# Performance work log

Hardware: AMD Instinct MI355X
Metric: run time of the kernel (lower is better)

The kernel has to match this reference:

```python
import jax, jax.numpy as jnp
import numpy as np

B, LS, LH, D1, D2 = 16, 1024, 1024, 1024, 1024


def setup_inputs() -> dict:
    key = jax.random.key(0)
    k1, k2, k3 = jax.random.split(key, 3)
    S = jax.random.normal(k1, (B, LS, D1), dtype=jnp.float32)
    H = jax.random.normal(k2, (B, LH, D2), dtype=jnp.float32)
    pad_mask = jnp.zeros((B, LS, LH), dtype=jnp.float32)  # additive mask
    W_w = jax.random.normal(k3, (D2, D1), dtype=jnp.float32) / np.sqrt(D1)
    W_b = jnp.zeros((D2,), dtype=jnp.float32)
    return {"S": S, "H": H, "pad_mask": pad_mask, "W_w": W_w, "W_b": W_b}


def reference(S, H, pad_mask, W_w, W_b):
    # Linear projection: S_ = S @ W^T + b  -> [B, LS, D2]
    S_ = jnp.einsum('bsd,ed->bse', S, W_w) + W_b
    # Unscaled dot-product scores: [B, LS, LH]
    score = jnp.einsum('bse,bte->bst', S_, H)
    score = score + pad_mask  # additive pad mask
    score = jax.nn.softmax(score, axis=-1)
    # Weighted sum of H: [B, LS, D2]
    out = jnp.einsum('bst,bte->bse', score, H)
    return out
```

## Files before the change

### kernel.cpp

```cpp
#include <hip/hip_runtime.h>
#include <stdint.h>

typedef _Float16 half8 __attribute__((ext_vector_type(8)));
typedef float floatx4 __attribute__((ext_vector_type(4)));

__device__ __forceinline__ uint16_t f16bits(_Float16 h) {
  union { _Float16 f; uint16_t u; } x; x.f = h; return x.u;
}

__device__ __forceinline__ void g2l16(const void* g, void* l) {
  __builtin_amdgcn_global_load_lds((const __attribute__((address_space(1))) void*)g,
                                   (__attribute__((address_space(3))) void*)l,
                                   16, 0, 0);
}

__global__ __launch_bounds__(256) void split_f16_kernel(
    const float* __restrict__ x, uint16_t* __restrict__ hi,
    uint16_t* __restrict__ lo, int n4) {
  int i = blockIdx.x * 256 + threadIdx.x;
  if (i >= n4) return;
  float4 v = ((const float4*)x)[i];
  ushort4 h, l;
  _Float16 a;
  a = (_Float16)v.x; h.x = f16bits(a); l.x = f16bits((_Float16)(v.x - (float)a));
  a = (_Float16)v.y; h.y = f16bits(a); l.y = f16bits((_Float16)(v.y - (float)a));
  a = (_Float16)v.z; h.z = f16bits(a); l.z = f16bits((_Float16)(v.z - (float)a));
  a = (_Float16)v.w; h.w = f16bits(a); l.w = f16bits((_Float16)(v.w - (float)a));
  ((ushort4*)hi)[i] = h;
  ((ushort4*)lo)[i] = l;
}

__global__ __launch_bounds__(256) void split_h_kernel(
    const float* __restrict__ src, uint16_t* __restrict__ hi,
    uint16_t* __restrict__ lo, uint16_t* __restrict__ ht) {
  __shared__ uint16_t tile[64][65];
  const int e0 = blockIdx.x * 64;
  const int t0 = blockIdx.y * 64;
  const size_t bb = (size_t)blockIdx.z << 20;
  const int r = threadIdx.x >> 4;
  const int c = (threadIdx.x & 15) * 4;
#pragma unroll
  for (int it = 0; it < 4; ++it) {
    const int tr = r + it * 16;
    const size_t idx = bb + (size_t)(t0 + tr) * 1024 + e0 + c;
    float4 v = *(const float4*)(src + idx);
    ushort4 h, l;
    _Float16 a;
    a = (_Float16)v.x; h.x = f16bits(a); l.x = f16bits((_Float16)(v.x - (float)a));
    a = (_Float16)v.y; h.y = f16bits(a); l.y = f16bits((_Float16)(v.y - (float)a));
    a = (_Float16)v.z; h.z = f16bits(a); l.z = f16bits((_Float16)(v.z - (float)a));
    a = (_Float16)v.w; h.w = f16bits(a); l.w = f16bits((_Float16)(v.w - (float)a));
    *(ushort4*)(hi + idx) = h;
    *(ushort4*)(lo + idx) = l;
    tile[c + 0][tr] = h.x;
    tile[c + 1][tr] = h.y;
    tile[c + 2][tr] = h.z;
    tile[c + 3][tr] = h.w;
  }
  __syncthreads();
#pragma unroll
  for (int it = 0; it < 4; ++it) {
    const int er = r + it * 16;
    ushort4 o;
    o.x = tile[er][c + 0];
    o.y = tile[er][c + 1];
    o.z = tile[er][c + 2];
    o.w = tile[er][c + 3];
    *(ushort4*)(ht + bb + (size_t)(e0 + er) * 1024 + t0 + c) = o;
  }
}

template <bool SPLIT, int MODE, int GMAP>
__global__ __launch_bounds__(256, 4) void gemm_bt(
    const uint16_t* __restrict__ Ahi, const uint16_t* __restrict__ Alo,
    const uint16_t* __restrict__ Bhi, const uint16_t* __restrict__ Blo,
    uint16_t* __restrict__ Chi, uint16_t* __restrict__ Clo,
    float* __restrict__ Cf, const float* __restrict__ mask,
    const float* __restrict__ bias, int N, int K,
    long batchA, long batchB, long batchC) {
  constexpr int NBUF = SPLIT ? 2 : 1;
  constexpr int LOI = SPLIT ? 1 : 0;
  __shared__ __align__(16) uint16_t sA[2][NBUF][128 * 32];
  __shared__ __align__(16) uint16_t sB[NBUF][128 * 32];

  const int tid = threadIdx.x;
  const int lane = tid & 63;
  const int w = tid >> 6;
  const int wr = w >> 1, wc = w & 1;
  const int quad = lane >> 4, l16 = lane & 15;

  int m_t, n_t, z;
  if constexpr (GMAP == 0) {
    m_t = blockIdx.x; n_t = blockIdx.y; z = 0;
  } else {
    z = blockIdx.x; m_t = blockIdx.y >> 3; n_t = blockIdx.y & 7;
  }
  const int m0 = m_t * 128;
  const int n0 = n_t * 128;
  const size_t zA = (size_t)z * batchA;
  const size_t zB = (size_t)z * batchB;
  const size_t zC = (size_t)z * batchC;

  const int r0 = w * 32 + (lane >> 2);
  const int ldc =
      (((lane & 3) ^ ((lane >> 2) & 3) ^ (((lane >> 4) & 1) << 1)) * 16);

  const char* gAh0 = (const char*)(Ahi + zA + (size_t)(m0 + r0) * K) + ldc;
  const char* gAh1 = gAh0 + (size_t)16 * K * 2;
  const char* gBh0 = (const char*)(Bhi + zB + (size_t)(n0 + r0) * K) + ldc;
  const char* gBh1 = gBh0 + (size_t)16 * K * 2;
  const char* gAl0 = gAh0; const char* gAl1 = gAh1;
  const char* gBl0 = gBh0; const char* gBl1 = gBh1;
  if constexpr (SPLIT) {
    gAl0 = (const char*)(Alo + zA + (size_t)(m0 + r0) * K) + ldc;
    gAl1 = gAl0 + (size_t)16 * K * 2;
    gBl0 = (const char*)(Blo + zB + (size_t)(n0 + r0) * K) + ldc;
    gBl1 = gBl0 + (size_t)16 * K * 2;
  }

  auto stageA = [&](int buf, int kt) {
    const int kb = kt * 64;
    g2l16(gAh0 + kb, &sA[buf][0][(w * 32) * 32]);
    g2l16(gAh1 + kb, &sA[buf][0][(w * 32 + 16) * 32]);
    if constexpr (SPLIT) {
      g2l16(gAl0 + kb, &sA[buf][LOI][(w * 32) * 32]);
      g2l16(gAl1 + kb, &sA[buf][LOI][(w * 32 + 16) * 32]);
    }
  };
  auto stageB = [&](int kt) {
    const int kb = kt * 64;
    g2l16(gBh0 + kb, &sB[0][(w * 32) * 32]);
    g2l16(gBh1 + kb, &sB[0][(w * 32 + 16) * 32]);
    if constexpr (SPLIT) {
      g2l16(gBl0 + kb, &sB[LOI][(w * 32) * 32]);
      g2l16(gBl1 + kb, &sB[LOI][(w * 32 + 16) * 32]);
    }
  };

  const int key = (l16 & 3) ^ (((l16 >> 2) & 1) << 1);
  const int aoff = (wr * 64 + l16) * 32 + ((quad ^ key) * 8);
  const int boff = (wc * 64 + l16) * 32 + ((quad ^ key) * 8);

  floatx4 acc[4][4];
  floatx4 zero = {0.f, 0.f, 0.f, 0.f};
#pragma unroll
  for (int i = 0; i < 4; ++i)
#pragma unroll
    for (int j = 0; j < 4; ++j) acc[i][j] = zero;

  const int nkt = K >> 5;
  stageA(0, 0);
  asm volatile("s_waitcnt vmcnt(0)" ::: "memory");
  __builtin_amdgcn_s_barrier();
  asm volatile("" ::: "memory");

  int cur = 0;
  for (int kt = 0; kt < nkt; ++kt) {
    stageB(kt);
    const bool pre = (kt + 1 < nkt);
    if (pre) stageA(cur ^ 1, kt + 1);

    half8 fa[4];
#pragma unroll
    for (int i = 0; i < 4; ++i) fa[i] = *(const half8*)&sA[cur][0][aoff + i * 512];

    if (pre) {
      if constexpr (SPLIT)
        asm volatile("s_waitcnt vmcnt(4)" ::: "memory");
      else
        asm volatile("s_waitcnt vmcnt(2)" ::: "memory");
    } else {
      asm volatile("s_waitcnt vmcnt(0)" ::: "memory");
    }
    __builtin_amdgcn_s_barrier();
    asm volatile("" ::: "memory");

    if constexpr (SPLIT) {
      half8 fbl[4];
#pragma unroll
      for (int j = 0; j < 4; ++j) fbl[j] = *(const half8*)&sB[1][boff + j * 512];
#pragma unroll
      for (int i = 0; i < 4; ++i)
#pragma unroll
        for (int j = 0; j < 4; ++j)
          acc[i][j] = __builtin_amdgcn_mfma_f32_16x16x32_f16(fa[i], fbl[j], acc[i][j], 0, 0, 0);
    }
    half8 fbh[4];
#pragma unroll
    for (int j = 0; j < 4; ++j) fbh[j] = *(const half8*)&sB[0][boff + j * 512];
#pragma unroll
    for (int i = 0; i < 4; ++i)
#pragma unroll
      for (int j = 0; j < 4; ++j)
        acc[i][j] = __builtin_amdgcn_mfma_f32_16x16x32_f16(fa[i], fbh[j], acc[i][j], 0, 0, 0);
    if constexpr (SPLIT) {
      half8 fal[4];
#pragma unroll
      for (int i = 0; i < 4; ++i) fal[i] = *(const half8*)&sA[cur][1][aoff + i * 512];
#pragma unroll
      for (int i = 0; i < 4; ++i)
#pragma unroll
        for (int j = 0; j < 4; ++j)
          acc[i][j] = __builtin_amdgcn_mfma_f32_16x16x32_f16(fal[i], fbh[j], acc[i][j], 0, 0, 0);
    }
    __syncthreads();
    cur ^= 1;
  }

  const int crow0 = m0 + wr * 64 + quad * 4;
  const int ccol0 = n0 + wc * 64 + l16;
#pragma unroll
  for (int j = 0; j < 4; ++j) {
    const int col = ccol0 + j * 16;
    float bj = 0.f;
    if constexpr (MODE == 0) bj = bias[col];
#pragma unroll
    for (int i = 0; i < 4; ++i) {
#pragma unroll
      for (int r = 0; r < 4; ++r) {
        const int row = crow0 + i * 16 + r;
        const size_t idx = zC + (size_t)row * N + col;
        float v = acc[i][j][r];
        if constexpr (MODE == 0) {
          v += bj;
          _Float16 h = (_Float16)v;
          Chi[idx] = f16bits(h);
          Clo[idx] = f16bits((_Float16)(v - (float)h));
        } else if constexpr (MODE == 1) {
          Cf[idx] = v + mask[idx];
        } else {
          Cf[idx] = v;
        }
      }
    }
  }
}

__global__ __launch_bounds__(256, 2) void gemm_bt_k64(
    const uint16_t* __restrict__ A, const uint16_t* __restrict__ B,
    float* __restrict__ Cf, int N, int K,
    long batchA, long batchB, long batchC) {
  __shared__ __align__(16) uint16_t sA[2][128 * 64];
  __shared__ __align__(16) uint16_t sB[2][128 * 64];

  const int tid = threadIdx.x;
  const int lane = tid & 63;
  const int w = tid >> 6;
  const int wr = w >> 1, wc = w & 1;
  const int quad = lane >> 4, l16 = lane & 15;

  const int z = blockIdx.x;
  const int m_t = blockIdx.y >> 3, n_t = blockIdx.y & 7;
  const int m0 = m_t * 128, n0 = n_t * 128;
  const size_t zA = (size_t)z * batchA;
  const size_t zB = (size_t)z * batchB;
  const size_t zC = (size_t)z * batchC;

  const int r0 = w * 32 + (lane >> 3);
  const int ldc = (((lane & 7) ^ ((lane >> 3) & 7)) * 16);
  const size_t rowskip = (size_t)8 * K * 2;

  const char* gA = (const char*)(A + zA + (size_t)(m0 + r0) * K) + ldc;
  const char* gB = (const char*)(B + zB + (size_t)(n0 + r0) * K) + ldc;

  auto stage = [&](int buf, int kt) {
    const int kb = kt * 128;
#pragma unroll
    for (int it = 0; it < 4; ++it) {
      g2l16(gA + it * rowskip + kb, &sA[buf][(w * 32 + it * 8) * 64]);
      g2l16(gB + it * rowskip + kb, &sB[buf][(w * 32 + it * 8) * 64]);
    }
  };

  const int key = l16 & 7;
  const int arow = wr * 64 + l16;
  const int brow = wc * 64 + l16;

  floatx4 acc[4][4];
  floatx4 zero = {0.f, 0.f, 0.f, 0.f};
#pragma unroll
  for (int i = 0; i < 4; ++i)
#pragma unroll
    for (int j = 0; j < 4; ++j) acc[i][j] = zero;

  const int nkt = K >> 6;
  stage(0, 0);
  __syncthreads();
  int cur = 0;
  for (int kt = 0; kt < nkt; ++kt) {
    if (kt + 1 < nkt) stage(cur ^ 1, kt + 1);
#pragma unroll
    for (int kh = 0; kh < 2; ++kh) {
      const int co = (((kh << 2) | quad) ^ key) * 8;
      half8 fa[4], fb[4];
#pragma unroll
      for (int i = 0; i < 4; ++i)
        fa[i] = *(const half8*)&sA[cur][(arow + 16 * i) * 64 + co];
#pragma unroll
      for (int j = 0; j < 4; ++j)
        fb[j] = *(const half8*)&sB[cur][(brow + 16 * j) * 64 + co];
#pragma unroll
      for (int i = 0; i < 4; ++i)
#pragma unroll
        for (int j = 0; j < 4; ++j)
          acc[i][j] = __builtin_amdgcn_mfma_f32_16x16x32_f16(fa[i], fb[j], acc[i][j], 0, 0, 0);
    }
    __syncthreads();
    cur ^= 1;
  }

  const int crow0 = m0 + wr * 64 + quad * 4;
  const int ccol0 = n0 + wc * 64 + l16;
#pragma unroll
  for (int j = 0; j < 4; ++j) {
    const int col = ccol0 + j * 16;
#pragma unroll
    for (int i = 0; i < 4; ++i) {
#pragma unroll
      for (int r = 0; r < 4; ++r) {
        const int row = crow0 + i * 16 + r;
        Cf[zC + (size_t)row * N + col] = acc[i][j][r];
      }
    }
  }
}

__global__ __launch_bounds__(256) void softmax_kernel(
    const float* __restrict__ sc, uint16_t* __restrict__ p) {
  const int row = blockIdx.x;
  const float* x = sc + (size_t)row * 1024;
  const int t = threadIdx.x;
  float4 v = ((const float4*)x)[t];
  float m = fmaxf(fmaxf(v.x, v.y), fmaxf(v.z, v.w));
#pragma unroll
  for (int off = 32; off; off >>= 1) m = fmaxf(m, __shfl_xor(m, off));
  __shared__ float redm[4];
  __shared__ float reds[4];
  const int wv = t >> 6, ln = t & 63;
  if (ln == 0) redm[wv] = m;
  __syncthreads();
  m = fmaxf(fmaxf(redm[0], redm[1]), fmaxf(redm[2], redm[3]));
  float e0 = __expf(v.x - m), e1 = __expf(v.y - m);
  float e2 = __expf(v.z - m), e3 = __expf(v.w - m);
  float s = e0 + e1 + e2 + e3;
#pragma unroll
  for (int off = 32; off; off >>= 1) s += __shfl_xor(s, off);
  if (ln == 0) reds[wv] = s;
  __syncthreads();
  s = reds[0] + reds[1] + reds[2] + reds[3];
  float inv = 1.f / s;
  ushort4 o;
  o.x = f16bits((_Float16)(e0 * inv));
  o.y = f16bits((_Float16)(e1 * inv));
  o.z = f16bits((_Float16)(e2 * inv));
  o.w = f16bits((_Float16)(e3 * inv));
  ((ushort4*)(p + (size_t)row * 1024))[t] = o;
}

__global__ __launch_bounds__(256) void transpose_f16_kernel(
    const float* __restrict__ src, uint16_t* __restrict__ dst) {
  __shared__ uint16_t tile[64][65];
  const int e0 = blockIdx.x * 64;
  const int t0 = blockIdx.y * 64;
  const size_t bb = (size_t)blockIdx.z << 20;
  const int r = threadIdx.x >> 4;
  const int c = (threadIdx.x & 15) * 4;
#pragma unroll
  for (int it = 0; it < 4; ++it) {
    const int tr = r + it * 16;
    float4 v = *(const float4*)(src + bb + (size_t)(t0 + tr) * 1024 + e0 + c);
    tile[c + 0][tr] = f16bits((_Float16)v.x);
    tile[c + 1][tr] = f16bits((_Float16)v.y);
    tile[c + 2][tr] = f16bits((_Float16)v.z);
    tile[c + 3][tr] = f16bits((_Float16)v.w);
  }
  __syncthreads();
#pragma unroll
  for (int it = 0; it < 4; ++it) {
    const int er = r + it * 16;
    ushort4 o;
    o.x = tile[er][c + 0];
    o.y = tile[er][c + 1];
    o.z = tile[er][c + 2];
    o.w = tile[er][c + 3];
    *(ushort4*)(dst + bb + (size_t)(e0 + er) * 1024 + t0 + c) = o;
  }
}

extern "C" void kernel_launch(void* const* d_in, const int* in_sizes, int n_in,
                              void* d_out, int out_size, void* d_ws, size_t ws_size,
                              hipStream_t stream) {
  (void)in_sizes; (void)n_in; (void)out_size;
  const float* S    = (const float*)d_in[0];
  const float* H    = (const float*)d_in[1];
  const float* mask = (const float*)d_in[2];
  const float* Ww   = (const float*)d_in[3];
  const float* Wb   = (const float*)d_in[4];
  float* out = (float*)d_out;
  char* ws = (char*)d_ws;
  const size_t MB = 1024ull * 1024ull;

  uint16_t* Whi  = (uint16_t*)(ws + 0 * MB);
  uint16_t* Wlo  = (uint16_t*)(ws + 2 * MB);
  uint16_t* Pjhi = (uint16_t*)(ws + 4 * MB);
  uint16_t* Pjlo = (uint16_t*)(ws + 36 * MB);
  uint16_t* Hhi  = (uint16_t*)(ws + 68 * MB);
  uint16_t* Hlo  = (uint16_t*)(ws + 100 * MB);
  uint16_t* Shi  = (uint16_t*)(ws + 132 * MB);
  uint16_t* Slo  = (uint16_t*)(ws + 164 * MB);
  float*    SC   = (float*)(ws + 132 * MB);
  uint16_t* PR   = (uint16_t*)(ws + 68 * MB);

  const bool roomy = ws_size >= 229ull * MB;
  uint16_t* HT = roomy ? (uint16_t*)(ws + 196 * MB)
                       : (uint16_t*)(ws + 100 * MB);

  split_f16_kernel<<<16384, 256, 0, stream>>>(S, Shi, Slo, 4 * 1024 * 1024);
  split_f16_kernel<<<1024, 256, 0, stream>>>(Ww, Whi, Wlo, 256 * 1024);
  if (roomy) {
    split_h_kernel<<<dim3(16, 16, 16), 256, 0, stream>>>(H, Hhi, Hlo, HT);
  } else {
    split_f16_kernel<<<16384, 256, 0, stream>>>(H, Hhi, Hlo, 4 * 1024 * 1024);
  }

  gemm_bt<true, 0, 0><<<dim3(128, 8, 1), 256, 0, stream>>>(
      Shi, Slo, Whi, Wlo, Pjhi, Pjlo, nullptr, nullptr, Wb,
      1024, 1024, 0, 0, 0);
  gemm_bt<true, 1, 1><<<dim3(16, 64, 1), 256, 0, stream>>>(
      Pjhi, Pjlo, Hhi, Hlo, nullptr, nullptr, SC, mask, nullptr,
      1024, 1024, 1048576, 1048576, 1048576);
  softmax_kernel<<<16384, 256, 0, stream>>>(SC, PR);
  if (!roomy) {
    transpose_f16_kernel<<<dim3(16, 16, 16), 256, 0, stream>>>(H, HT);
  }
  gemm_bt_k64<<<dim3(16, 64, 1), 256, 0, stream>>>(
      PR, HT, out, 1024, 1024, 1048576, 1048576, 1048576);
}
```

Baseline: 509.7 us.

## Fuse the fp32 S hi/lo split into the projection GEMM's load path

Removes the separate split kernel that converted S into f16 hi/lo buffers. A new projection GEMM reads fp32 S directly, splits it into hi/lo halves in registers and writes them into swizzled LDS. The fp32 loads are software-pipelined with manual vmcnt waits and a raw s_barrier. This cuts a full read-write pass over S in global memory. The dedicated K64 output GEMM is dropped, and the final P@H GEMM now uses the generic gemm_bt template, which may be slower for that stage.

```diff
diff --git a/kernel.cpp b/kernel.cpp
--- a/kernel.cpp
+++ b/kernel.cpp
@@ -236,12 +236,13 @@
   }
 }
 
-__global__ __launch_bounds__(256, 2) void gemm_bt_k64(
-    const uint16_t* __restrict__ A, const uint16_t* __restrict__ B,
-    float* __restrict__ Cf, int N, int K,
-    long batchA, long batchB, long batchC) {
-  __shared__ __align__(16) uint16_t sA[2][128 * 64];
-  __shared__ __align__(16) uint16_t sB[2][128 * 64];
+__global__ __launch_bounds__(256, 2) void gemm1_fused(
+    const float* __restrict__ Af, const uint16_t* __restrict__ Bhi,
+    const uint16_t* __restrict__ Blo, uint16_t* __restrict__ Chi,
+    uint16_t* __restrict__ Clo, const float* __restrict__ bias,
+    int N, int K) {
+  __shared__ __align__(16) uint16_t sA[2][2][128 * 32];
+  __shared__ __align__(16) uint16_t sB[2][128 * 32];
 
   const int tid = threadIdx.x;
   const int lane = tid & 63;
@@ -249,32 +250,54 @@
   const int wr = w >> 1, wc = w & 1;
   const int quad = lane >> 4, l16 = lane & 15;
 
-  const int z = blockIdx.x;
-  const int m_t = blockIdx.y >> 3, n_t = blockIdx.y & 7;
-  const int m0 = m_t * 128, n0 = n_t * 128;
-  const size_t zA = (size_t)z * batchA;
-  const size_t zB = (size_t)z * batchB;
-  const size_t zC = (size_t)z * batchC;
-
-  const int r0 = w * 32 + (lane >> 3);
-  const int ldc = (((lane & 7) ^ ((lane >> 3) & 7)) * 16);
-  const size_t rowskip = (size_t)8 * K * 2;
-
-  const char* gA = (const char*)(A + zA + (size_t)(m0 + r0) * K) + ldc;
-  const char* gB = (const char*)(B + zB + (size_t)(n0 + r0) * K) + ldc;
-
-  auto stage = [&](int buf, int kt) {
-    const int kb = kt * 128;
+  const int m0 = blockIdx.x * 128;
+  const int n0 = blockIdx.y * 128;
+
+  const int r0 = w * 32 + (lane >> 2);
+  const int ldc =
+      (((lane & 3) ^ ((lane >> 2) & 3) ^ (((lane >> 4) & 1) << 1)) * 16);
+  const char* gBh0 = (const char*)(Bhi + (size_t)(n0 + r0) * K) + ldc;
+  const char* gBh1 = gBh0 + (size_t)16 * K * 2;
+  const char* gBl0 = (const char*)(Blo + (size_t)(n0 + r0) * K) + ldc;
+  const char* gBl1 = gBl0 + (size_t)16 * K * 2;
+  auto stageB = [&](int kt) {
+    const int kb = kt * 64;
+    g2l16(gBh0 + kb, &sB[0][(w * 32) * 32]);
+    g2l16(gBh1 + kb, &sB[0][(w * 32 + 16) * 32]);
+    g2l16(gBl0 + kb, &sB[1][(w * 32) * 32]);
+    g2l16(gBl1 + kb, &sB[1][(w * 32 + 16) * 32]);
+  };
+
+  const int ra8 = lane >> 3;
+  const int c32 = lane & 7;
+  const int keyA = (ra8 & 3) ^ (((ra8 >> 2) & 1) << 1);
+  const int wsl = ((c32 >> 1) ^ keyA) * 8 + (c32 & 1) * 4;
+  const float* gA = Af + (size_t)(m0 + w * 32 + ra8) * K + c32 * 4;
+
+  float4 av[4];
+  auto issueA = [&](int kt) {
+#pragma unroll
+    for (int it = 0; it < 4; ++it)
+      av[it] = *(const float4*)(gA + (size_t)it * 8 * K + kt * 32);
+  };
+  auto writeA = [&](int buf) {
 #pragma unroll
     for (int it = 0; it < 4; ++it) {
-      g2l16(gA + it * rowskip + kb, &sA[buf][(w * 32 + it * 8) * 64]);
-      g2l16(gB + it * rowskip + kb, &sB[buf][(w * 32 + it * 8) * 64]);
+      ushort4 hh, ll;
+      _Float16 a;
+      a = (_Float16)av[it].x; hh.x = f16bits(a); ll.x = f16bits((_Float16)(av[it].x - (float)a));
+      a = (_Float16)av[it].y; hh.y = f16bits(a); ll.y = f16bits((_Float16)(av[it].y - (float)a));
+      a = (_Float16)av[it].z; hh.z = f16bits(a); ll.z = f16bits((_Float16)(av[it].z - (float)a));
+      a = (_Float16)av[it].w; hh.w = f16bits(a); ll.w = f16bits((_Float16)(av[it].w - (float)a));
+      const int off = (w * 32 + ra8 + 8 * it) * 32 + wsl;
+      *(ushort4*)&sA[buf][0][off] = hh;
+      *(ushort4*)&sA[buf][1][off] = ll;
     }
   };
 
-  const int key = l16 & 7;
-  const int arow = wr * 64 + l16;
-  const int brow = wc * 64 + l16;
+  const int key = (l16 & 3) ^ (((l16 >> 2) & 1) << 1);
+  const int aoff = (wr * 64 + l16) * 32 + ((quad ^ key) * 8);
+  const int boff = (wc * 64 + l16) * 32 + ((quad ^ key) * 8);
 
   floatx4 acc[4][4];
   floatx4 zero = {0.f, 0.f, 0.f, 0.f};
@@ -283,28 +306,56 @@
 #pragma unroll
     for (int j = 0; j < 4; ++j) acc[i][j] = zero;
 
-  const int nkt = K >> 6;
-  stage(0, 0);
+  const int nkt = K >> 5;
+  issueA(0);
+  writeA(0);
   __syncthreads();
+
   int cur = 0;
   for (int kt = 0; kt < nkt; ++kt) {
-    if (kt + 1 < nkt) stage(cur ^ 1, kt + 1);
-#pragma unroll
-    for (int kh = 0; kh < 2; ++kh) {
-      const int co = (((kh << 2) | quad) ^ key) * 8;
-      half8 fa[4], fb[4];
+    stageB(kt);
+    asm volatile("" ::: "memory");
+    const bool pre = (kt + 1 < nkt);
+    if (pre) issueA(kt + 1);
+
+    half8 fa[4];
+#pragma unroll
+    for (int i = 0; i < 4; ++i) fa[i] = *(const half8*)&sA[cur][0][aoff + i * 512];
+
+    if (pre) asm volatile("s_waitcnt vmcnt(4)" ::: "memory");
+    else     asm volatile("s_waitcnt vmcnt(0)" ::: "memory");
+    __builtin_amdgcn_s_barrier();
+    asm volatile("" ::: "memory");
+
+    {
+      half8 fbl[4];
+#pragma unroll
+      for (int j = 0; j < 4; ++j) fbl[j] = *(const half8*)&sB[1][boff + j * 512];
 #pragma unroll
       for (int i = 0; i < 4; ++i)
-        fa[i] = *(const half8*)&sA[cur][(arow + 16 * i) * 64 + co];
+#pragma unroll
+        for (int j = 0; j < 4; ++j)
+          acc[i][j] = __builtin_amdgcn_mfma_f32_16x16x32_f16(fa[i], fbl[j], acc[i][j], 0, 0, 0);
+    }
+    half8 fbh[4];
+#pragma unroll
+    for (int j = 0; j < 4; ++j) fbh[j] = *(const half8*)&sB[0][boff + j * 512];
+#pragma unroll
+    for (int i = 0; i < 4; ++i)
 #pragma unroll
       for (int j = 0; j < 4; ++j)
-        fb[j] = *(const half8*)&sB[cur][(brow + 16 * j) * 64 + co];
+        acc[i][j] = __builtin_amdgcn_mfma_f32_16x16x32_f16(fa[i], fbh[j], acc[i][j], 0, 0, 0);
+    {
+      half8 fal[4];
+#pragma unroll
+      for (int i = 0; i < 4; ++i) fal[i] = *(const half8*)&sA[cur][1][aoff + i * 512];
 #pragma unroll
       for (int i = 0; i < 4; ++i)
 #pragma unroll
         for (int j = 0; j < 4; ++j)
-          acc[i][j] = __builtin_amdgcn_mfma_f32_16x16x32_f16(fa[i], fb[j], acc[i][j], 0, 0, 0);
-    }
+          acc[i][j] = __builtin_amdgcn_mfma_f32_16x16x32_f16(fal[i], fbh[j], acc[i][j], 0, 0, 0);
+    }
+    if (pre) writeA(cur ^ 1);
     __syncthreads();
     cur ^= 1;
   }
@@ -314,12 +365,17 @@
 #pragma unroll
   for (int j = 0; j < 4; ++j) {
     const int col = ccol0 + j * 16;
+    const float bj = bias[col];
 #pragma unroll
     for (int i = 0; i < 4; ++i) {
 #pragma unroll
       for (int r = 0; r < 4; ++r) {
         const int row = crow0 + i * 16 + r;
-        Cf[zC + (size_t)row * N + col] = acc[i][j][r];
+        const size_t idx = (size_t)row * N + col;
+        float v = acc[i][j][r] + bj;
+        _Float16 h = (_Float16)v;
+        Chi[idx] = f16bits(h);
+        Clo[idx] = f16bits((_Float16)(v - (float)h));
       }
     }
   }
@@ -406,8 +462,6 @@
   uint16_t* Pjlo = (uint16_t*)(ws + 36 * MB);
   uint16_t* Hhi  = (uint16_t*)(ws + 68 * MB);
   uint16_t* Hlo  = (uint16_t*)(ws + 100 * MB);
-  uint16_t* Shi  = (uint16_t*)(ws + 132 * MB);
-  uint16_t* Slo  = (uint16_t*)(ws + 164 * MB);
   float*    SC   = (float*)(ws + 132 * MB);
   uint16_t* PR   = (uint16_t*)(ws + 68 * MB);
 
@@ -415,7 +469,6 @@
   uint16_t* HT = roomy ? (uint16_t*)(ws + 196 * MB)
                        : (uint16_t*)(ws + 100 * MB);
 
-  split_f16_kernel<<<16384, 256, 0, stream>>>(S, Shi, Slo, 4 * 1024 * 1024);
   split_f16_kernel<<<1024, 256, 0, stream>>>(Ww, Whi, Wlo, 256 * 1024);
   if (roomy) {
     split_h_kernel<<<dim3(16, 16, 16), 256, 0, stream>>>(H, Hhi, Hlo, HT);
@@ -423,9 +476,8 @@
     split_f16_kernel<<<16384, 256, 0, stream>>>(H, Hhi, Hlo, 4 * 1024 * 1024);
   }
 
-  gemm_bt<true, 0, 0><<<dim3(128, 8, 1), 256, 0, stream>>>(
-      Shi, Slo, Whi, Wlo, Pjhi, Pjlo, nullptr, nullptr, Wb,
-      1024, 1024, 0, 0, 0);
+  gemm1_fused<<<dim3(128, 8, 1), 256, 0, stream>>>(
+      S, Whi, Wlo, Pjhi, Pjlo, Wb, 1024, 1024);
   gemm_bt<true, 1, 1><<<dim3(16, 64, 1), 256, 0, stream>>>(
       Pjhi, Pjlo, Hhi, Hlo, nullptr, nullptr, SC, mask, nullptr,
       1024, 1024, 1048576, 1048576, 1048576);
@@ -433,6 +485,7 @@
   if (!roomy) {
     transpose_f16_kernel<<<dim3(16, 16, 16), 256, 0, stream>>>(H, HT);
   }
-  gemm_bt_k64<<<dim3(16, 64, 1), 256, 0, stream>>>(
-      PR, HT, out, 1024, 1024, 1048576, 1048576, 1048576);
-}
+  gemm_bt<false, 2, 1><<<dim3(16, 64, 1), 256, 0, stream>>>(
+      PR, nullptr, HT, nullptr, nullptr, nullptr, out, nullptr, nullptr,
+      1024, 1024, 1048576, 1048576, 1048576);
+}
```

New measurement: 510.5 us. Within noise of the previous version (+0.2%).
